# Kernel optimization log

Hardware: AMD Instinct MI355X
Metric: run time of the kernel (lower is better)

The kernel has to match this reference:

```python
import jax, jax.numpy as jnp
import numpy as np

T, V, E, H = 512, 32000, 512, 512

def setup_inputs() -> dict:
    key = jax.random.key(0)
    ks = jax.random.split(key, 6)
    return {
        "sent": jax.random.normal(ks[0], (T, V), dtype=jnp.float32),
        "W_e": jax.random.normal(ks[1], (E, V), dtype=jnp.float32),
        "W_x": jax.random.normal(ks[2], (H, E), dtype=jnp.float32),
        "W_h": jax.random.normal(ks[3], (H, H), dtype=jnp.float32),
        "W_p": jax.random.normal(ks[4], (V, H), dtype=jnp.float32),
        "b": jax.random.normal(ks[5], (H,), dtype=jnp.float32),
    }

def reference(sent, W_e, W_x, W_h, W_p, b):
    # Embed all input words at once (embed_word: W_e @ word), skip last token.
    emb = sent[:-1] @ W_e.T                 # [T-1, E]
    xproj = emb @ W_x.T + b                 # [T-1, H] (W_x @ e + b precomputed)

    def step(h_prev, xp):
        h = jax.nn.sigmoid(xp + W_h @ h_prev)  # elman_unit
        return h, h

    h0 = jnp.zeros((H,), dtype=jnp.float32)
    _, hs = jax.lax.scan(step, h0, xproj)   # [T-1, H]
    logits = hs @ W_p.T                     # [T-1, V]
    preds = jax.nn.softmax(logits, axis=-1) # softmax over vocab (dim=0 per step)
    return preds
```

## Files before the change

### kernel.cpp

```cpp
#include <hip/hip_runtime.h>
#include <math.h>

#define ROWS 511
#define VV   32000
#define HH   512

#define RDEP    3
#define SLOTF   3584
#define NLW     14
#define DARRCAP 26112
#define TBL     520

__device__ __forceinline__ int pad4not8(int x) {
    int p = (x + 3) & ~3;
    if ((p & 7) == 0) p += 4;
    return p;
}
__device__ __forceinline__ int pad4(int x) { return (x + 3) & ~3; }

__device__ __forceinline__ void gld_lds16(const float* g, float* l) {
    __builtin_amdgcn_global_load_lds(
        (const __attribute__((address_space(1))) void*)g,
        (__attribute__((address_space(3))) void*)l, 16, 0, 0);
}

__global__ __launch_bounds__(256) void gemm_nt(
    const float* __restrict__ A, const float* __restrict__ B, float* __restrict__ C,
    int M, int lda, int ldb, int ldc, int kChunk, int useAtomic)
{
    __shared__ float As[16][68];
    __shared__ float Bs[16][68];
    const int tid = threadIdx.x;
    const int bn = blockIdx.x, bm = blockIdx.y, bz = blockIdx.z;
    const int row = tid >> 2;
    const int seg = (tid & 3) << 2;
    const int tm  = (tid >> 4) << 2;
    const int tn  = (tid & 15) << 2;
    const int am = bm*64 + row;
    const size_t k0 = (size_t)bz * kChunk;
    const float* Ap = A + (size_t)am*lda + k0 + seg;
    const float* Bp = B + (size_t)(bn*64 + row)*ldb + k0 + seg;
    const bool aok = (am < M);
    float acc[4][4];
#pragma unroll
    for (int i=0;i<4;i++)
#pragma unroll
        for (int j=0;j<4;j++) acc[i][j]=0.f;

    for (int kt = 0; kt < kChunk; kt += 16) {
        float4 av = aok ? *(const float4*)(Ap + kt) : make_float4(0.f,0.f,0.f,0.f);
        float4 bv = *(const float4*)(Bp + kt);
        __syncthreads();
        As[seg+0][row]=av.x; As[seg+1][row]=av.y; As[seg+2][row]=av.z; As[seg+3][row]=av.w;
        Bs[seg+0][row]=bv.x; Bs[seg+1][row]=bv.y; Bs[seg+2][row]=bv.z; Bs[seg+3][row]=bv.w;
        __syncthreads();
#pragma unroll
        for (int k=0;k<16;k++){
            const float4 a  = *(const float4*)&As[k][tm];
            const float4 b4 = *(const float4*)&Bs[k][tn];
            float ar[4]={a.x,a.y,a.z,a.w};
            float br[4]={b4.x,b4.y,b4.z,b4.w};
#pragma unroll
            for (int i=0;i<4;i++)
#pragma unroll
                for (int j=0;j<4;j++)
                    acc[i][j] += ar[i]*br[j];
        }
    }
#pragma unroll
    for (int i=0;i<4;i++){
        int gm = bm*64 + tm + i;
        if (gm < M) {
            float* Cp = C + (size_t)gm*ldc + bn*64 + tn;
            if (useAtomic) {
                atomicAdd(Cp+0, acc[i][0]); atomicAdd(Cp+1, acc[i][1]);
                atomicAdd(Cp+2, acc[i][2]); atomicAdd(Cp+3, acc[i][3]);
            } else {
                *(float4*)Cp = make_float4(acc[i][0],acc[i][1],acc[i][2],acc[i][3]);
            }
        }
    }
}

__global__ __launch_bounds__(64) void rsum_kernel(const float* __restrict__ W_h, float* __restrict__ R)
{
    const int j = blockIdx.x;
    const int lane = threadIdx.x;
    float s = 0.f;
    for (int i = lane; i < HH; i += 64) s += fabsf(W_h[(size_t)j*HH + i]);
#pragma unroll
    for (int off = 32; off >= 1; off >>= 1) s += __shfl_down(s, off);
    if (lane == 0) R[j] = s;
}

__global__ __launch_bounds__(512) void classify_kernel(
    float* __restrict__ xp, const float* __restrict__ b, const float* __restrict__ R,
    float* __restrict__ Hm, int* __restrict__ idxJ, int* __restrict__ cnt)
{
    const int t = blockIdx.x;
    const int j = threadIdx.x;
    __shared__ int c;
    if (j == 0) c = 0;
    __syncthreads();
    float v = xp[(size_t)t*HH + j] + b[j];
    xp[(size_t)t*HH + j] = v;
    Hm[(size_t)t*HH + j] = (v > 0.f) ? 1.f : 0.f;
    if (fabsf(v) < R[j] + 30.0f) {
        int slot = atomicAdd(&c, 1);
        if (slot < 128) idxJ[t*128 + slot] = j;
    }
    __syncthreads();
    if (j == 0) cnt[t] = (c < 128) ? c : 128;
}

__global__ __launch_bounds__(512) void prefix_kernel(
    const int* __restrict__ cnt, int* __restrict__ offs, int* __restrict__ d4offs)
{
    __shared__ int sA[512];
    __shared__ int sB[512];
    const int t = threadIdx.x;
    int a = 0, b = 0;
    if (t >= 1 && t <= 510) a = cnt[t] * pad4not8(cnt[t-1]);
    if (t <= 510) b = pad4(cnt[t]);
    sA[t] = a; sB[t] = b;
    int va = a, vb = b;
    __syncthreads();
    for (int d = 1; d < 512; d <<= 1) {
        int ua = (t >= d) ? sA[t-d] : 0;
        int ub = (t >= d) ? sB[t-d] : 0;
        __syncthreads();
        va += ua; vb += ub;
        sA[t] = va; sB[t] = vb;
        __syncthreads();
    }
    if (t <= 510) offs[t] = va - a;
    d4offs[t] = vb - b;
}

__global__ __launch_bounds__(256) void gather_kernel(
    const float* __restrict__ W_h, const float* __restrict__ xp, const float* __restrict__ U,
    const int* __restrict__ idxJ, const int* __restrict__ cnt, const int* __restrict__ offs,
    float* __restrict__ wsub, int wsub_cap, float2* __restrict__ zs)
{
    const int t = blockIdx.x;
    const int cj = cnt[t];
    for (int jj = threadIdx.x; jj < cj; jj += 256) {
        int j = idxJ[t*128 + jj];
        float xpv = xp[(size_t)t*HH + j];
        float v = xpv;
        if (t > 0) v += U[(size_t)(t-1)*HH + j];
        zs[t*128 + jj] = make_float2(v, (xpv > 0.f) ? 1.f : 0.f);
    }
    if (t == 0) return;
    const int ci  = cnt[t-1];
    const int cip = pad4not8(ci);
    const int nw  = cj * cip;
    const int base = offs[t];
    if (base + nw > wsub_cap) return;
    for (int r = 0; r < cj; ++r) {
        const float* Wrow = W_h + (size_t)idxJ[t*128 + r] * HH;
        for (int c = threadIdx.x; c < cip; c += 256)
            wsub[base + r*cip + c] = (c < ci) ? Wrow[idxJ[(t-1)*128 + c]] : 0.f;
    }
}

__global__ __launch_bounds__(64) void scan_kernel(
    const float2* __restrict__ zs, const int* __restrict__ idxJ,
    const int* __restrict__ cnt, const int* __restrict__ offs, const int* __restrict__ d4offs,
    const float* __restrict__ wsub, int wsub_cap,
    const float* __restrict__ W_h, float* __restrict__ Hm, float* __restrict__ darrg)
{
    __shared__ __align__(16) float  ring[RDEP * SLOTF];
    __shared__ __align__(16) float2 zsr[RDEP * 128];
    __shared__ __align__(16) float  darr[DARRCAP];
    __shared__ __align__(16) float  db[2][132];
    __shared__ int scnt[TBL], soffs[TBL], sd4[TBL];
    const int lane = threadIdx.x;

    for (int i = lane; i < TBL; i += 64) {
        scnt[i]  = (i < ROWS) ? cnt[i]  : 0;
        soffs[i] = (i < ROWS) ? offs[i] : 0;
        sd4[i]   = (i < ROWS) ? d4offs[i] : d4offs[511];
    }
    for (int i = lane * 4; i < DARRCAP; i += 256)
        *(float4*)&darr[i] = make_float4(0.f, 0.f, 0.f, 0.f);
    for (int i = lane; i < 132; i += 64) { db[0][i] = 0.f; db[1][i] = 0.f; }
    __syncthreads();

    const int  total   = sd4[511];
    const bool useDarr = (total <= DARRCAP - 64);

    {
        const int cj0 = scnt[0];
        for (int jj = lane; jj < cj0; jj += 64) {
            float2 zz = zs[jj];
            float h = 1.f / (1.f + __expf(-zz.x));
            float d = h - zz.y;
            if (useDarr) darr[jj] = d;
            else { db[0][jj] = d; Hm[idxJ[jj]] = h; }
        }
    }

    for (int s = 1; s <= RDEP; ++s) {
        const int slot = s % RDEP;
        int wb = soffs[s];
        int sb = (wb + SLOTF <= wsub_cap) ? wb : 0;
        const float* gw = wsub + sb + lane * 4;
        float* lw = &ring[slot * SLOTF];
#pragma unroll
        for (int k = 0; k < NLW; ++k)
            gld_lds16(gw + k * 256, lw + k * 256);
        const float* gz = (const float*)(zs + (size_t)s * 128) + lane * 4;
        gld_lds16(gz, (float*)&zsr[slot * 128]);
    }

    for (int t = 1; t <= 510; ++t) {
        const int slot = t % RDEP;
        const int cj   = scnt[t];
        const int ci   = scnt[t-1];
        const int cip  = pad4not8(ci);
        const int nw   = cj * cip;
        const int wb   = soffs[t];
        const bool fast = (cj <= 64) && (nw <= SLOTF) && (wb + SLOTF <= wsub_cap);
        const float* dvec = useDarr ? &darr[sd4[t-1]] : db[(t-1) & 1];

        asm volatile("s_waitcnt vmcnt(30)" ::: "memory");

        float2 zc = make_float2(0.f, 0.f);
        float  z  = 0.f;
        if (fast && lane < cj) {
            zc = zsr[slot * 128 + lane];
            z  = zc.x;
            const float4* wr = (const float4*)&ring[slot * SLOTF + lane * cip];
            const float4* dr = (const float4*)dvec;
            const int n4 = cip >> 2;
            float a0 = 0.f, a1 = 0.f, a2 = 0.f, a3 = 0.f;
            for (int q = 0; q < n4; ++q) {
                float4 w = wr[q];
                float4 d = dr[q];
                a0 += w.x * d.x; a1 += w.y * d.y;
                a2 += w.z * d.z; a3 += w.w * d.w;
            }
            z += (a0 + a1) + (a2 + a3);
        }

        asm volatile("s_waitcnt lgkmcnt(0)" ::: "memory");
        {
            const int tn = t + RDEP;
            int wb2 = soffs[tn];
            int sb = (wb2 + SLOTF <= wsub_cap) ? wb2 : 0;
            const float* gw = wsub + sb + lane * 4;
            float* lw = &ring[slot * SLOTF];
#pragma unroll
            for (int k = 0; k < NLW; ++k)
                gld_lds16(gw + k * 256, lw + k * 256);
            const float* gz = (const float*)(zs + (size_t)tn * 128) + lane * 4;
            gld_lds16(gz, (float*)&zsr[slot * 128]);
        }

        if (fast) {
            if (lane < cj) {
                float h = 1.f / (1.f + __expf(-z));
                float d = h - zc.y;
                if (useDarr) darr[sd4[t] + lane] = d;
                else { db[t & 1][lane] = d; Hm[(size_t)t*HH + idxJ[t*128 + lane]] = h; }
            }
        } else {
            for (int jj = lane; jj < cj; jj += 64) {
                int j = idxJ[t*128 + jj];
                float2 zz = zs[(size_t)t*128 + jj];
                float zv = zz.x;
                for (int ii = 0; ii < ci; ++ii)
                    zv += W_h[(size_t)j*HH + idxJ[(t-1)*128 + ii]] * dvec[ii];
                float h = 1.f / (1.f + __expf(-zv));
                float d = h - zz.y;
                if (useDarr) darr[sd4[t] + jj] = d;
                else { db[t & 1][jj] = d; Hm[(size_t)t*HH + j] = h; }
            }
        }
    }

    if (useDarr) {
        for (int i = lane * 4; i < total; i += 256)
            *(float4*)&darrg[i] = *(float4*)&darr[i];
    }
}

__global__ __launch_bounds__(64) void scatter_kernel(
    const float2* __restrict__ zs, const int* __restrict__ idxJ,
    const int* __restrict__ cnt, const int* __restrict__ d4offs,
    const float* __restrict__ darrg, float* __restrict__ Hm)
{
    if (d4offs[511] > DARRCAP - 64) return;
    const int t = blockIdx.x;
    const int c = cnt[t];
    for (int jj = threadIdx.x; jj < c; jj += 64)
        Hm[(size_t)t*HH + idxJ[t*128 + jj]] = zs[(size_t)t*128 + jj].y + darrg[d4offs[t] + jj];
}

__global__ __launch_bounds__(256) void softmax_kernel(float* __restrict__ out)
{
    const int row = blockIdx.x;
    const int tid = threadIdx.x;
    float* p = out + (size_t)row * VV;
    float m = -INFINITY, l = 0.f;
    for (int i = tid; i < VV; i += 256) {
        float x = p[i];
        if (x > m) { l = l * __expf(m - x) + 1.f; m = x; }
        else       { l += __expf(x - m); }
    }
#pragma unroll
    for (int off = 32; off >= 1; off >>= 1) {
        float m2 = __shfl_down(m, off);
        float l2 = __shfl_down(l, off);
        float M  = fmaxf(m, m2);
        l = l * __expf(m - M) + l2 * __expf(m2 - M);
        m = M;
    }
    __shared__ float sm[4], sl[4];
    const int wid = tid >> 6, lane = tid & 63;
    if (lane == 0) { sm[wid] = m; sl[wid] = l; }
    __syncthreads();
    if (tid == 0) {
        float M = sm[0], L = sl[0];
        for (int w = 1; w < 4; ++w) {
            float M2 = fmaxf(M, sm[w]);
            L = L * __expf(M - M2) + sl[w] * __expf(sm[w] - M2);
            M = M2;
        }
        sm[0] = M; sl[0] = 1.0f / L;
    }
    __syncthreads();
    const float M = sm[0], inv = sl[0];
    for (int i = tid; i < VV; i += 256) p[i] = __expf(p[i] - M) * inv;
}

extern "C" void kernel_launch(void* const* d_in, const int* in_sizes, int n_in,
                              void* d_out, int out_size, void* d_ws, size_t ws_size,
                              hipStream_t stream)
{
    const float* sent = (const float*)d_in[0];
    const float* W_e  = (const float*)d_in[1];
    const float* W_x  = (const float*)d_in[2];
    const float* W_h  = (const float*)d_in[3];
    const float* W_p  = (const float*)d_in[4];
    const float* b    = (const float*)d_in[5];
    float* out = (float*)d_out;
    float* ws  = (float*)d_ws;

    float*  emb    = ws;
    float*  xp     = ws + 262144;
    float*  U      = ws + 524288;
    float*  Hm     = ws + 786432;
    float*  R      = ws + 1048576;
    int*    cnt    = (int*)(ws + 1049088);
    int*    idxJ   = (int*)(ws + 1049600);
    int*    offs   = (int*)(ws + 1115136);
    int*    d4offs = (int*)(ws + 1115648);
    float2* zs     = (float2*)(ws + 1116160);
    float*  darrg  = ws + 1246976;
    float*  wsub   = ws + 1273088;
    long avail = (long)(ws_size / 4) - 1273088;
    int wsub_cap = (avail > 8388608L) ? 8388608 : (avail > 0 ? (int)avail : 0);

    hipMemsetAsync(ws, 0, (size_t)786432 * sizeof(float), stream);

    rsum_kernel<<<512, 64, 0, stream>>>(W_h, R);

    gemm_nt<<<dim3(8, 8, 8), 256, 0, stream>>>(sent, W_e, emb, ROWS, VV, VV, HH, 4000, 1);
    gemm_nt<<<dim3(8, 8, 4), 256, 0, stream>>>(emb, W_x, xp, ROWS, HH, HH, HH, 128, 1);

    classify_kernel<<<ROWS, 512, 0, stream>>>(xp, b, R, Hm, idxJ, cnt);

    gemm_nt<<<dim3(8, 8, 4), 256, 0, stream>>>(Hm, W_h, U, ROWS, HH, HH, HH, 128, 1);

    prefix_kernel<<<1, 512, 0, stream>>>(cnt, offs, d4offs);
    gather_kernel<<<ROWS, 256, 0, stream>>>(W_h, xp, U, idxJ, cnt, offs, wsub, wsub_cap, zs);
    scan_kernel<<<1, 64, 0, stream>>>(zs, idxJ, cnt, offs, d4offs, wsub, wsub_cap, W_h, Hm, darrg);
    scatter_kernel<<<ROWS, 64, 0, stream>>>(zs, idxJ, cnt, d4offs, darrg, Hm);

    gemm_nt<<<dim3(500, 8, 1), 256, 0, stream>>>(Hm, W_p, out, ROWS, HH, HH, VV, 512, 0);
    softmax_kernel<<<ROWS, 256, 0, stream>>>(out);
}
```

Measured before the change: 1.390 ms.

## Prefetch recurrent weight rows into registers with double-buffered scan pipeline

Replaces the LDS ring buffer filled by global_load_lds with per-lane register double buffers (WA/WB) that prefetch the next step's weight row and z values straight from global memory while the current step computes. The per-step tables are packed into one int4 record and read through readfirstlane so the scalars stay uniform. The intent is to take LDS round-trips and waitcnt stalls off the serial recurrence critical path. The cost is higher VGPR use, since up to 34 float4 registers are held, and only one step of lookahead instead of three, which may expose global load latency.

```diff
diff --git a/kernel.cpp b/kernel.cpp
--- a/kernel.cpp
+++ b/kernel.cpp
@@ -5,11 +5,10 @@
 #define VV   32000
 #define HH   512
 
-#define RDEP    3
 #define SLOTF   3584
-#define NLW     14
 #define DARRCAP 26112
 #define TBL     520
+#define MAXQ    17
 
 __device__ __forceinline__ int pad4not8(int x) {
     int p = (x + 3) & ~3;
@@ -18,11 +17,7 @@
 }
 __device__ __forceinline__ int pad4(int x) { return (x + 3) & ~3; }
 
-__device__ __forceinline__ void gld_lds16(const float* g, float* l) {
-    __builtin_amdgcn_global_load_lds(
-        (const __attribute__((address_space(1))) void*)g,
-        (__attribute__((address_space(3))) void*)l, 16, 0, 0);
-}
+__device__ __forceinline__ int rfl(int x) { return __builtin_amdgcn_readfirstlane(x); }
 
 __global__ __launch_bounds__(256) void gemm_nt(
     const float* __restrict__ A, const float* __restrict__ B, float* __restrict__ C,
@@ -170,28 +165,28 @@
     const float* __restrict__ wsub, int wsub_cap,
     const float* __restrict__ W_h, float* __restrict__ Hm, float* __restrict__ darrg)
 {
-    __shared__ __align__(16) float  ring[RDEP * SLOTF];
-    __shared__ __align__(16) float2 zsr[RDEP * 128];
     __shared__ __align__(16) float  darr[DARRCAP];
     __shared__ __align__(16) float  db[2][132];
-    __shared__ int scnt[TBL], soffs[TBL], sd4[TBL];
+    __shared__ __align__(16) int4   rec[TBL];
     const int lane = threadIdx.x;
+    const float* zsf = (const float*)zs;
 
     for (int i = lane; i < TBL; i += 64) {
-        scnt[i]  = (i < ROWS) ? cnt[i]  : 0;
-        soffs[i] = (i < ROWS) ? offs[i] : 0;
-        sd4[i]   = (i < ROWS) ? d4offs[i] : d4offs[511];
+        int c = (i < ROWS) ? cnt[i]    : 0;
+        int o = (i < ROWS) ? offs[i]   : 0;
+        int d = (i < ROWS) ? d4offs[i] : d4offs[511];
+        rec[i] = make_int4(c, o, d, 0);
     }
     for (int i = lane * 4; i < DARRCAP; i += 256)
         *(float4*)&darr[i] = make_float4(0.f, 0.f, 0.f, 0.f);
     for (int i = lane; i < 132; i += 64) { db[0][i] = 0.f; db[1][i] = 0.f; }
     __syncthreads();
 
-    const int  total   = sd4[511];
+    const int  total   = rfl(rec[511].z);
     const bool useDarr = (total <= DARRCAP - 64);
 
     {
-        const int cj0 = scnt[0];
+        const int cj0 = rfl(rec[0].x);
         for (int jj = lane; jj < cj0; jj += 64) {
             float2 zz = zs[jj];
             float h = 1.f / (1.f + __expf(-zz.x));
@@ -201,82 +196,106 @@
         }
     }
 
-    for (int s = 1; s <= RDEP; ++s) {
-        const int slot = s % RDEP;
-        int wb = soffs[s];
-        int sb = (wb + SLOTF <= wsub_cap) ? wb : 0;
-        const float* gw = wsub + sb + lane * 4;
-        float* lw = &ring[slot * SLOTF];
-#pragma unroll
-        for (int k = 0; k < NLW; ++k)
-            gld_lds16(gw + k * 256, lw + k * 256);
-        const float* gz = (const float*)(zs + (size_t)s * 128) + lane * 4;
-        gld_lds16(gz, (float*)&zsr[slot * 128]);
-    }
-
-    for (int t = 1; t <= 510; ++t) {
-        const int slot = t % RDEP;
-        const int cj   = scnt[t];
-        const int ci   = scnt[t-1];
-        const int cip  = pad4not8(ci);
-        const int nw   = cj * cip;
-        const int wb   = soffs[t];
-        const bool fast = (cj <= 64) && (nw <= SLOTF) && (wb + SLOTF <= wsub_cap);
-        const float* dvec = useDarr ? &darr[sd4[t-1]] : db[(t-1) & 1];
-
-        asm volatile("s_waitcnt vmcnt(30)" ::: "memory");
-
-        float2 zc = make_float2(0.f, 0.f);
-        float  z  = 0.f;
-        if (fast && lane < cj) {
-            zc = zsr[slot * 128 + lane];
-            z  = zc.x;
-            const float4* wr = (const float4*)&ring[slot * SLOTF + lane * cip];
-            const float4* dr = (const float4*)dvec;
-            const int n4 = cip >> 2;
-            float a0 = 0.f, a1 = 0.f, a2 = 0.f, a3 = 0.f;
-            for (int q = 0; q < n4; ++q) {
-                float4 w = wr[q];
-                float4 d = dr[q];
-                a0 += w.x * d.x; a1 += w.y * d.y;
-                a2 += w.z * d.z; a3 += w.w * d.w;
-            }
-            z += (a0 + a1) + (a2 + a3);
-        }
-
-        asm volatile("s_waitcnt lgkmcnt(0)" ::: "memory");
+    float4 WA[MAXQ], WB[MAXQ];
+    float2 zA, zB;
+
+    int ciP, sd4P;
+    int cjC, sd4C, n4C;
+    bool fastC;
+    int cjN, wbN, sd4N;
+    int n4N; bool fastN;
+    int4 rnNN;
+
+#define PREFETCH(TT1, NXTW, ZN) do {                                            \
+        int cipN_ = pad4not8(cjC);                                              \
+        n4N = cipN_ >> 2;                                                       \
+        fastN = (cjN <= 64) && (cipN_ <= 68) &&                                 \
+                ((long)cjN * cipN_ <= SLOTF) && (wbN + SLOTF <= wsub_cap);      \
+        int rowN_ = min(lane, max(cjN - 1, 0));                                 \
+        const float* gW_ = wsub + (fastN ? (wbN + rowN_ * cipN_) : 0);          \
+        _Pragma("unroll")                                                       \
+        for (int q = 0; q < MAXQ; ++q) {                                        \
+            int off_ = (q < n4N) ? (q << 2) : 0;                                \
+            NXTW[q] = *(const float4*)(gW_ + off_);                             \
+        }                                                                       \
+        ZN = *(const float2*)&zsf[(size_t)(TT1) * 256 + (lane << 1)];           \
+    } while (0)
+
+#define COMPUTE(TT, CURW, ZC) do {                                              \
+        const float* dvec_ = useDarr ? &darr[sd4P] : db[((TT) - 1) & 1];        \
+        if (fastC) {                                                            \
+            if (lane < cjC) {                                                   \
+                const float4* dr_ = (const float4*)dvec_;                       \
+                float4 Dv[MAXQ];                                                \
+                _Pragma("unroll")                                               \
+                for (int g = 0; g < MAXQ; g += 4) {                             \
+                    if (g < n4C) {                                              \
+                        _Pragma("unroll")                                       \
+                        for (int q = g; q < g + 4 && q < MAXQ; ++q)             \
+                            Dv[q] = dr_[q];                                     \
+                    }                                                           \
+                }                                                               \
+                float a0 = 0.f, a1 = 0.f, a2 = 0.f, a3 = 0.f;                   \
+                _Pragma("unroll")                                               \
+                for (int q = 0; q < MAXQ; ++q) {                                \
+                    if (q < n4C) {                                              \
+                        a0 += CURW[q].x * Dv[q].x; a1 += CURW[q].y * Dv[q].y;   \
+                        a2 += CURW[q].z * Dv[q].z; a3 += CURW[q].w * Dv[q].w;   \
+                    }                                                           \
+                }                                                               \
+                float z = ZC.x + (a0 + a1) + (a2 + a3);                         \
+                float h = 1.f / (1.f + __expf(-z));                             \
+                float d = h - ZC.y;                                             \
+                if (useDarr) darr[sd4C + lane] = d;                             \
+                else { db[(TT) & 1][lane] = d;                                  \
+                       Hm[(size_t)(TT)*HH + idxJ[(TT)*128 + lane]] = h; }       \
+            }                                                                   \
+        } else {                                                                \
+            for (int jj = lane; jj < cjC; jj += 64) {                           \
+                int j = idxJ[(TT)*128 + jj];                                    \
+                float2 zz = zs[(size_t)(TT)*128 + jj];                          \
+                float zv = zz.x;                                                \
+                for (int ii = 0; ii < ciP; ++ii)                                \
+                    zv += W_h[(size_t)j*HH + idxJ[((TT)-1)*128 + ii]] * dvec_[ii]; \
+                float h = 1.f / (1.f + __expf(-zv));                            \
+                float dd = h - zz.y;                                            \
+                if (useDarr) darr[sd4C + jj] = dd;                              \
+                else { db[(TT) & 1][jj] = dd;                                   \
+                       Hm[(size_t)(TT)*HH + j] = h; }                           \
+            }                                                                   \
+        }                                                                       \
+    } while (0)
+
+#define ROTATE(RN3) do {                                                        \
+        ciP = cjC; sd4P = sd4C;                                                 \
+        cjC = cjN; sd4C = sd4N; fastC = fastN; n4C = n4N;                       \
+        cjN = rfl(rnNN.x); wbN = rfl(rnNN.y); sd4N = rfl(rnNN.z);               \
+        rnNN = (RN3);                                                           \
+    } while (0)
+
+    ciP  = rfl(rec[0].x);
+    sd4P = rfl(rec[0].z);
+    cjC  = ciP;
+    cjN  = rfl(rec[1].x);
+    wbN  = rfl(rec[1].y);
+    sd4N = rfl(rec[1].z);
+    PREFETCH(1, WA, zA);
+    cjC = cjN; sd4C = sd4N; fastC = fastN; n4C = n4N;
+    cjN = rfl(rec[2].x); wbN = rfl(rec[2].y); sd4N = rfl(rec[2].z);
+    rnNN = rec[3];
+
+    for (int t = 1; t <= 510; t += 2) {
         {
-            const int tn = t + RDEP;
-            int wb2 = soffs[tn];
-            int sb = (wb2 + SLOTF <= wsub_cap) ? wb2 : 0;
-            const float* gw = wsub + sb + lane * 4;
-            float* lw = &ring[slot * SLOTF];
-#pragma unroll
-            for (int k = 0; k < NLW; ++k)
-                gld_lds16(gw + k * 256, lw + k * 256);
-            const float* gz = (const float*)(zs + (size_t)tn * 128) + lane * 4;
-            gld_lds16(gz, (float*)&zsr[slot * 128]);
-        }
-
-        if (fast) {
-            if (lane < cj) {
-                float h = 1.f / (1.f + __expf(-z));
-                float d = h - zc.y;
-                if (useDarr) darr[sd4[t] + lane] = d;
-                else { db[t & 1][lane] = d; Hm[(size_t)t*HH + idxJ[t*128 + lane]] = h; }
-            }
-        } else {
-            for (int jj = lane; jj < cj; jj += 64) {
-                int j = idxJ[t*128 + jj];
-                float2 zz = zs[(size_t)t*128 + jj];
-                float zv = zz.x;
-                for (int ii = 0; ii < ci; ++ii)
-                    zv += W_h[(size_t)j*HH + idxJ[(t-1)*128 + ii]] * dvec[ii];
-                float h = 1.f / (1.f + __expf(-zv));
-                float d = h - zz.y;
-                if (useDarr) darr[sd4[t] + jj] = d;
-                else { db[t & 1][jj] = d; Hm[(size_t)t*HH + j] = h; }
-            }
+            PREFETCH(t + 1, WB, zB);
+            int4 rn3 = rec[t + 3];
+            COMPUTE(t, WA, zA);
+            ROTATE(rn3);
+        }
+        {
+            PREFETCH(t + 2, WA, zA);
+            int4 rn3 = rec[t + 4];
+            COMPUTE(t + 1, WB, zB);
+            ROTATE(rn3);
         }
     }
 
@@ -284,6 +303,9 @@
         for (int i = lane * 4; i < total; i += 256)
             *(float4*)&darrg[i] = *(float4*)&darr[i];
     }
+#undef PREFETCH
+#undef COMPUTE
+#undef ROTATE
 }
 
 __global__ __launch_bounds__(64) void scatter_kernel(
```

After: 1.213 ms. -12.7%, faster.
